# Optimization experiments

Measured on AMD Instinct MI355X. Metric: run time of the kernel, lower is better.

## Reference

```python
import jax, jax.numpy as jnp
import numpy as np

N, R, E, H, F = 50000, 6, 32768, 256, 16
NH, HD = 8, 32
EPS_LN = 1e-5

def _ln(x, g, b):
    mu = x.mean(-1, keepdims=True)
    var = ((x - mu) ** 2).mean(-1, keepdims=True)
    return (x - mu) * jax.lax.rsqrt(var + EPS_LN) * g + b

def setup_inputs() -> dict:
    key = jax.random.key(0)
    ks = jax.random.split(key, 32)
    s = lambda i, shape, scale=0.05: jax.random.normal(ks[i], shape, jnp.float32) * scale
    return {
        'x': jax.random.normal(ks[0], (N, H), jnp.float32),
        'edge_index': jax.random.randint(ks[1], (R, 2, E), 0, N, jnp.int32),
        'edge_attr': jax.random.normal(ks[2], (R, E, F), jnp.float32),
        'Wq': s(3, (R, H, H)), 'bq': s(4, (R, H)),
        'Wk': s(5, (R, H + F, H)), 'bk': s(6, (R, H)),
        'Wv': s(7, (R, H + F, H)), 'bv': s(8, (R, H)),
        'prior': jnp.ones((R, NH), jnp.float32),
        'Wm': s(9, (R, H, H)), 'bm': s(10, (R, H)),
        'W_ir1': s(11, (R * H, H)), 'b_ir1': s(12, (H,)),
        'W_ir2': s(13, (H, R)), 'b_ir2': s(14, (R,)),
        'Wmp': s(15, (3, H, H)), 'bmp': s(16, (3, H)),
        'Wa1': s(17, (H, H // 2)), 'ba1': s(18, (H // 2,)),
        'Wa2': s(19, (H // 2, 1)),
        'g_meta': jnp.ones((H,), jnp.float32), 'b_meta': jnp.zeros((H,), jnp.float32),
        'Wc': s(20, (2 * H, H)), 'bc': s(21, (H,)),
        'g_out': jnp.ones((H,), jnp.float32), 'b_out': jnp.zeros((H,), jnp.float32),
    }

def _block(x, edge_index, edge_attr, Wq, bq, Wk, bk, Wv, bv, prior, Wm, bm,
           W_ir1, b_ir1, W_ir2, b_ir2, Wmp, bmp, Wa1, ba1, Wa2, g_meta, b_meta,
           Wc, bc, g_out, b_out):
    def rel_layer(eidx, eattr, wq, bq_, wk, bk_, wv, bv_, pr, wm, bm_):
        src, dst = eidx[0], eidx[1]
        q = x @ wq + bq_                                  # [N,H]
        kv_in = jnp.concatenate([x[src], eattr], -1)      # [E,H+F]
        k = (kv_in @ wk + bk_).reshape(E, NH, HD)
        v = (kv_in @ wv + bv_).reshape(E, NH, HD)
        qe = q[dst].reshape(E, NH, HD)
        scores = (qe * k).sum(-1) / np.sqrt(HD) * pr      # [E,NH]
        m = jax.ops.segment_max(scores, dst, num_segments=N)
        ex = jnp.exp(scores - m[dst])
        denom = jax.ops.segment_sum(ex, dst, num_segments=N)
        w = ex / (denom[dst] + 1e-16)
        wv_flat = (w[..., None] * v).reshape(E, H)
        agg = jax.ops.segment_sum(wv_flat, dst, num_segments=N)  # [N,H]
        return jax.nn.gelu(agg @ wm + bm_, approximate=False)

    rel_out = jax.vmap(rel_layer)(edge_index, edge_attr, Wq, bq, Wk, bk, Wv, bv,
                                  prior, Wm, bm)          # [R,N,H]

    all_rel = jnp.transpose(rel_out, (1, 0, 2)).reshape(N, R * H)
    h = jax.nn.gelu(all_rel @ W_ir1 + b_ir1, approximate=False)
    inter_w = jax.nn.softmax(h @ W_ir2 + b_ir2, axis=-1)  # [N,R]
    inter_agg = jnp.einsum('nr,rnh->nh', inter_w, rel_out)

    # meta-paths: 0=entangle(ENTANGLE=2,SWAP=3) 1=control(CONTROL=4,ROTATION=0) 2=local(PAULI=1,TEMPORAL=5)
    paths = jnp.stack([rel_out[2] + rel_out[3], rel_out[4] + rel_out[0],
                       rel_out[1] + rel_out[5]], axis=1)  # [N,3,H]
    stacked = jnp.einsum('nph,phk->npk', paths, Wmp) + bmp
    attn = jax.nn.softmax((jnp.tanh(stacked @ Wa1 + ba1) @ Wa2).squeeze(-1), axis=1)
    meta = _ln((attn[..., None] * stacked).sum(1), g_meta, b_meta)

    combined = jax.nn.gelu(jnp.concatenate([inter_agg, meta], -1) @ Wc + bc,
                           approximate=False)
    return _ln(x + combined, g_out, b_out)

def reference(x, edge_index, edge_attr, Wq, bq, Wk, bk, Wv, bv, prior, Wm, bm,
              W_ir1, b_ir1, W_ir2, b_ir2, Wmp, bmp, Wa1, ba1, Wa2, g_meta, b_meta,
              Wc, bc, g_out, b_out):
    return _block(x, edge_index, edge_attr, Wq, bq, Wk, bk, Wv, bv, prior, Wm, bm,
                  W_ir1, b_ir1, W_ir2, b_ir2, Wmp, bmp, Wa1, ba1, Wa2,
                  g_meta, b_meta, Wc, bc, g_out, b_out)
```

## Files before the change

kernel.cpp:

```cpp
#include <hip/hip_runtime.h>
#include <hip/hip_bf16.h>

typedef __hip_bfloat16 bf16;
typedef __attribute__((ext_vector_type(8))) short short8;
typedef __attribute__((ext_vector_type(4))) float f32x4;

#define NN 50000
#define RR 6
#define EE 32768
#define HH 256
#define FF 16
#define NHEAD 8
#define KVP 320

struct __align__(8) bf16x4 { bf16 v[4]; };

__device__ __forceinline__ float b2f(bf16 v) { return __bfloat162float(v); }
__device__ __forceinline__ bf16 f2b(float v) { return __float2bfloat16(v); }
__device__ __forceinline__ short f2s(float f) { bf16 b = f2b(f); return __builtin_bit_cast(short, b); }
__device__ __forceinline__ float s2f(short s) { return b2f(__builtin_bit_cast(bf16, s)); }
__device__ __forceinline__ float gelu_f(float x) { return 0.5f * x * (1.0f + erff(x * 0.7071067811865476f)); }
__device__ __forceinline__ unsigned fkey(float f) { unsigned u = __float_as_uint(f); return (u & 0x80000000u) ? ~u : (u | 0x80000000u); }
__device__ __forceinline__ float fdec(unsigned k) { unsigned u = (k & 0x80000000u) ? (k & 0x7fffffffu) : ~k; return __uint_as_float(u); }

__device__ __forceinline__ void gl2lds16(const void* g, void* l) {
  __builtin_amdgcn_global_load_lds(
      (const __attribute__((address_space(1))) unsigned int*)g,
      (__attribute__((address_space(3))) unsigned int*)l, 16, 0, 0);
}

__global__ void zero_k(uint4* __restrict__ p, int n16)
{
  const uint4 z = make_uint4(0u, 0u, 0u, 0u);
  for (int i = blockIdx.x * blockDim.x + threadIdx.x; i < n16; i += gridDim.x * blockDim.x)
    p[i] = z;
}

__global__ void cvt_k(const float* __restrict__ in, bf16* __restrict__ out, int n4)
{
  const int i = blockIdx.x * 256 + threadIdx.x;
  if (i >= n4) return;
  const float4 f = ((const float4*)in)[i];
  bf16x4 o; o.v[0] = f2b(f.x); o.v[1] = f2b(f.y); o.v[2] = f2b(f.z); o.v[3] = f2b(f.w);
  ((bf16x4*)out)[i] = o;
}

__global__ void tconv_k(const float* __restrict__ in, bf16* __restrict__ out,
                        int K, int NC, int Kp, long izs, long ozs)
{
  __shared__ float t[32][33];
  in  += (size_t)blockIdx.z * izs;
  out += (size_t)blockIdx.z * ozs;
  const int kb = blockIdx.x * 32, nb = blockIdx.y * 32;
  const int tx = threadIdx.x & 31, ty = threadIdx.x >> 5;
  for (int i = ty; i < 32; i += 8) {
    const int k = kb + i, n = nb + tx;
    t[i][tx] = (k < K && n < NC) ? in[(size_t)k * NC + n] : 0.f;
  }
  __syncthreads();
  for (int i = ty; i < 32; i += 8) {
    const int n = nb + i, k = kb + tx;
    if (n < NC && k < Kp) out[(size_t)n * Kp + k] = f2b(t[tx][i]);
  }
}

__global__ void bkv_k(const float* __restrict__ bk, const float* __restrict__ bv,
                      float* __restrict__ bkv)
{
  const int i = blockIdx.x * 256 + threadIdx.x;
  if (i >= RR * 512) return;
  const int r = i >> 9, c = i & 511;
  bkv[i] = (c < 256) ? bk[r * 256 + c] : bv[r * 256 + (c - 256)];
}

__global__ void copyslot_k(const bf16* __restrict__ tmp, bf16* __restrict__ slot)
{
  const int i = blockIdx.x * 256 + threadIdx.x;
  if (i >= NN * 32) return;
  const int n = i >> 5, c = (i & 31) * 8;
  *(short8*)(slot + (size_t)n * 1536 + c) = *(const short8*)(tmp + (size_t)n * 256 + c);
}

template<int ASRC, int ACT, int ZMODE, typename TO>
__global__ __launch_bounds__(256) void mm_k(
    const void* __restrict__ Av, const bf16* __restrict__ A2, int lda,
    const int* __restrict__ src, const float* __restrict__ eattr,
    const bf16* __restrict__ Bt, const float* __restrict__ bias,
    const float* __restrict__ wa2, TO* __restrict__ C, int ldc,
    float* __restrict__ logits, int M, int K, int z0)
{
  __shared__ short lA[128 * 64];
  __shared__ short lB[128 * 64];
  const int tid = threadIdx.x;
  const int w = tid >> 6, l = tid & 63;
  const int col0 = blockIdx.x << 7;
  const int row0 = blockIdx.y << 7;
  const bf16* Ab = (const bf16*)Av;
  const bf16* A2b = A2;
  const bf16* Btz = Bt;
  const float* biasz = bias;
  TO* Cz = C;
  float* lg = logits;
  if constexpr (ZMODE == 1) {
    const int slots3[3] = {2, 4, 1};
    Ab = (const bf16*)Av + slots3[blockIdx.z] * 256;
    lg = logits + (size_t)blockIdx.z * M;
  } else if constexpr (ZMODE == 3) {
    const int r1s[3] = {2, 4, 1}, r2s[3] = {3, 0, 5};
    const int z = blockIdx.z + z0;
    Ab  = (const bf16*)Av + (size_t)r1s[z] * 256;
    A2b = A2 + (size_t)r2s[z] * 256;
    Btz = Bt + (size_t)z * 256 * K;
    biasz = bias + z * 256;
    Cz = C + (size_t)blockIdx.z * (size_t)M * 256;
  }
  const int wm = (w >> 1) << 6, wn = (w & 1) << 6;
  const int lane15 = l & 15, kq = l >> 4;

  f32x4 acc[4][4] = {};

  for (int k0 = 0; k0 < K; k0 += 64) {
#pragma unroll
    for (int i = 0; i < 4; ++i) {
      const int idx = (w * 4 + i) * 64 + l;
      const int row = idx >> 3, cg = idx & 7;
      const int scg = cg ^ (row & 7);
      const int r = min(row0 + row, M - 1);
      const int kc = k0 + scg * 8;
      if constexpr (ASRC == 0) {
        gl2lds16(Ab + (size_t)r * lda + kc, &lA[idx * 8]);
      } else if constexpr (ASRC == 2) {
        const short8 u  = *(const short8*)(Ab + (size_t)r * lda + kc);
        const short8 v2 = *(const short8*)(A2b + (size_t)r * lda + kc);
        short8 s;
#pragma unroll
        for (int j = 0; j < 8; ++j) s[j] = f2s(s2f(u[j]) + s2f(v2[j]));
        *(short8*)&lA[idx * 8] = s;
      } else {
        short8 s;
        if (kc < HH) {
          s = *(const short8*)((const bf16*)Av + (size_t)src[r] * HH + kc);
        } else if (kc < HH + FF) {
          const float* p = eattr + (size_t)r * FF + (kc - HH);
          const float4 f0 = *(const float4*)p;
          const float4 f1 = *(const float4*)(p + 4);
          s[0] = f2s(f0.x); s[1] = f2s(f0.y); s[2] = f2s(f0.z); s[3] = f2s(f0.w);
          s[4] = f2s(f1.x); s[5] = f2s(f1.y); s[6] = f2s(f1.z); s[7] = f2s(f1.w);
        } else {
#pragma unroll
          for (int j = 0; j < 8; ++j) s[j] = 0;
        }
        *(short8*)&lA[idx * 8] = s;
      }
    }
#pragma unroll
    for (int i = 0; i < 4; ++i) {
      const int idx = (w * 4 + i) * 64 + l;
      const int row = idx >> 3, cg = idx & 7;
      const int scg = cg ^ (row & 7);
      gl2lds16(Btz + (size_t)(col0 + row) * K + k0 + scg * 8, &lB[idx * 8]);
    }
    __syncthreads();
#pragma unroll
    for (int kk = 0; kk < 64; kk += 32) {
      short8 af[4], bfr[4];
#pragma unroll
      for (int t = 0; t < 4; ++t) {
        const int ra = wm + t * 16 + lane15;
        const int ca = ((kk >> 3) + kq) ^ (ra & 7);
        af[t] = *(const short8*)&lA[ra * 64 + ca * 8];
        const int rb = wn + t * 16 + lane15;
        const int cb = ((kk >> 3) + kq) ^ (rb & 7);
        bfr[t] = *(const short8*)&lB[rb * 64 + cb * 8];
      }
#pragma unroll
      for (int ti = 0; ti < 4; ++ti)
#pragma unroll
        for (int tj = 0; tj < 4; ++tj)
          acc[ti][tj] = __builtin_amdgcn_mfma_f32_16x16x32_bf16(af[ti], bfr[tj], acc[ti][tj], 0, 0, 0);
    }
    __syncthreads();
  }

  if constexpr (ZMODE != 1) {
#pragma unroll
    for (int ti = 0; ti < 4; ++ti) {
#pragma unroll
      for (int reg = 0; reg < 4; ++reg) {
        const int row = row0 + wm + ti * 16 + kq * 4 + reg;
        if (row >= M) continue;
#pragma unroll
        for (int tj = 0; tj < 4; ++tj) {
          const int col = col0 + wn + tj * 16 + lane15;
          float v = acc[ti][tj][reg] + biasz[col];
          if constexpr (ACT == 1) v = gelu_f(v);
          if constexpr (sizeof(TO) == 2) Cz[(size_t)row * ldc + col] = (TO)f2b(v);
          else                           Cz[(size_t)row * ldc + col] = (TO)v;
        }
      }
    }
  } else {
#pragma unroll
    for (int ti = 0; ti < 4; ++ti) {
#pragma unroll
      for (int reg = 0; reg < 4; ++reg) {
        float part = 0.f;
#pragma unroll
        for (int tj = 0; tj < 4; ++tj) {
          const int col = col0 + wn + tj * 16 + lane15;
          part += tanhf(acc[ti][tj][reg] + biasz[col]) * wa2[col];
        }
#pragma unroll
        for (int off = 8; off > 0; off >>= 1) part += __shfl_xor(part, off, 64);
        const int row = row0 + wm + ti * 16 + kq * 4 + reg;
        if (lane15 == 0 && row < M) atomicAdd(&lg[row], part);
      }
    }
  }
}

__global__ void scores_k(const bf16* __restrict__ q, const bf16* __restrict__ kv,
                         const int* __restrict__ dst_idx, const float* __restrict__ prior_r,
                         float* __restrict__ scores, unsigned* __restrict__ mkey)
{
  const int e = blockIdx.x, t = threadIdx.x;
  const int dst = dst_idx[e];
  float p = b2f(q[(size_t)dst * 1536 + t]) * b2f(kv[(size_t)e * 512 + t]);
#pragma unroll
  for (int off = 16; off > 0; off >>= 1) p += __shfl_down(p, off, 32);
  const int h = t >> 5;
  if ((t & 31) == 0) {
    const float s = p * 0.1767766952966369f * prior_r[h];
    scores[e * NHEAD + h] = s;
    atomicMax(&mkey[dst * NHEAD + h], fkey(s));
  }
}

__global__ void expden_k(const float* __restrict__ scores, const int* __restrict__ dst_idx,
                         const unsigned* __restrict__ mkey, float* __restrict__ ex,
                         float* __restrict__ denom)
{
  const int idx = blockIdx.x * 256 + threadIdx.x;
  if (idx >= EE * NHEAD) return;
  const int e = idx >> 3, h = idx & 7;
  const int dst = dst_idx[e];
  const float m = fdec(mkey[dst * NHEAD + h]);
  const float v = expf(scores[idx] - m);
  ex[idx] = v;
  atomicAdd(&denom[dst * NHEAD + h], v);
}

__global__ void agg_k(const float* __restrict__ ex, const float* __restrict__ denom,
                      const bf16* __restrict__ kv, const int* __restrict__ dst_idx,
                      float* __restrict__ agg)
{
  const int e = blockIdx.x, t = threadIdx.x, h = t >> 5;
  const int dst = dst_idx[e];
  const float w = ex[e * NHEAD + h] / (denom[dst * NHEAD + h] + 1e-16f);
  atomicAdd(&agg[(size_t)dst * HH + t], w * b2f(kv[(size_t)e * 512 + 256 + t]));
}

__global__ void interw_k(const bf16* __restrict__ h, const float* __restrict__ W2,
                         const float* __restrict__ b2, float* __restrict__ interw)
{
  const int wv = threadIdx.x >> 6, ln = threadIdx.x & 63;
  const int n = blockIdx.x * 4 + wv;
  if (n >= NN) return;
  float a[6] = {0.f, 0.f, 0.f, 0.f, 0.f, 0.f};
#pragma unroll
  for (int kq = 0; kq < 4; ++kq) {
    const int k = ln + (kq << 6);
    const float hv = b2f(h[(size_t)n * HH + k]);
#pragma unroll
    for (int j = 0; j < 6; ++j) a[j] += hv * W2[k * 6 + j];
  }
#pragma unroll
  for (int j = 0; j < 6; ++j) {
#pragma unroll
    for (int off = 32; off > 0; off >>= 1) a[j] += __shfl_down(a[j], off, 64);
  }
  if (ln == 0) {
    float lg[6], e[6], mx = -1e30f, s = 0.f;
#pragma unroll
    for (int j = 0; j < 6; ++j) { lg[j] = a[j] + b2[j]; mx = fmaxf(mx, lg[j]); }
#pragma unroll
    for (int j = 0; j < 6; ++j) { e[j] = expf(lg[j] - mx); s += e[j]; }
    const float inv = 1.0f / s;
#pragma unroll
    for (int j = 0; j < 6; ++j) interw[(size_t)n * 6 + j] = e[j] * inv;
  }
}

__global__ void interagg_k(const float* __restrict__ interw, const bf16* __restrict__ rel_cat,
                           bf16* __restrict__ comb)
{
  const int n = blockIdx.x, t = threadIdx.x;
  float acc = 0.f;
#pragma unroll
  for (int r = 0; r < 6; ++r)
    acc += interw[(size_t)n * 6 + r] * b2f(rel_cat[(size_t)n * 1536 + r * 256 + t]);
  comb[(size_t)n * 512 + t] = f2b(acc);
}

__global__ void metafinal_k(const float* __restrict__ logits, const bf16* __restrict__ rel_cat,
                            const float* __restrict__ gmeta, const float* __restrict__ bmeta,
                            bf16* __restrict__ comb)
{
  const int wv = threadIdx.x >> 6, ln = threadIdx.x & 63;
  const int n = blockIdx.x * 4 + wv;
  if (n >= NN) return;
  const float l0 = logits[n], l1 = logits[NN + n], l2 = logits[2 * NN + n];
  const float mx = fmaxf(l0, fmaxf(l1, l2));
  const float e0 = expf(l0 - mx), e1 = expf(l1 - mx), e2 = expf(l2 - mx);
  const float inv = 1.0f / (e0 + e1 + e2);
  const float a0 = e0 * inv, a1 = e1 * inv, a2 = e2 * inv;
  const size_t base = (size_t)n * 1536;
  float pre[4], s = 0.f, s2 = 0.f;
#pragma unroll
  for (int q4 = 0; q4 < 4; ++q4) {
    const int j = ln + (q4 << 6);
    const float v = a0 * b2f(rel_cat[base + 2 * 256 + j])
                  + a1 * b2f(rel_cat[base + 4 * 256 + j])
                  + a2 * b2f(rel_cat[base + 1 * 256 + j]);
    pre[q4] = v; s += v; s2 += v * v;
  }
#pragma unroll
  for (int off = 32; off > 0; off >>= 1) { s += __shfl_down(s, off, 64); s2 += __shfl_down(s2, off, 64); }
  s = __shfl(s, 0, 64); s2 = __shfl(s2, 0, 64);
  const float mu = s * (1.0f / 256.0f);
  const float var = s2 * (1.0f / 256.0f) - mu * mu;
  const float rs = rsqrtf(var + 1e-5f);
#pragma unroll
  for (int q4 = 0; q4 < 4; ++q4) {
    const int j = ln + (q4 << 6);
    comb[(size_t)n * 512 + 256 + j] = f2b((pre[q4] - mu) * rs * gmeta[j] + bmeta[j]);
  }
}

__global__ void final_k(const float* __restrict__ x, const float* __restrict__ combined,
                        const float* __restrict__ g, const float* __restrict__ b,
                        float* __restrict__ out)
{
  __shared__ float sred[8];
  const int n = blockIdx.x, t = threadIdx.x;
  const float v = x[(size_t)n * HH + t] + combined[(size_t)n * HH + t];
  float s = v, s2 = v * v;
#pragma unroll
  for (int off = 32; off > 0; off >>= 1) { s += __shfl_down(s, off, 64); s2 += __shfl_down(s2, off, 64); }
  const int wv = t >> 6;
  if ((t & 63) == 0) { sred[wv] = s; sred[4 + wv] = s2; }
  __syncthreads();
  const float st = sred[0] + sred[1] + sred[2] + sred[3];
  const float st2 = sred[4] + sred[5] + sred[6] + sred[7];
  const float mu = st * (1.0f / 256.0f);
  const float var = st2 * (1.0f / 256.0f) - mu * mu;
  const float rs = rsqrtf(var + 1e-5f);
  out[(size_t)n * HH + t] = (v - mu) * rs * g[t] + b[t];
}

extern "C" void kernel_launch(void* const* d_in, const int* in_sizes, int n_in,
                              void* d_out, int out_size, void* d_ws, size_t ws_size,
                              hipStream_t stream)
{
  const float* x      = (const float*)d_in[0];
  const int*   eidx   = (const int*)d_in[1];
  const float* eattr  = (const float*)d_in[2];
  const float* Wq     = (const float*)d_in[3];
  const float* bq     = (const float*)d_in[4];
  const float* Wk     = (const float*)d_in[5];
  const float* bk     = (const float*)d_in[6];
  const float* Wv     = (const float*)d_in[7];
  const float* bv     = (const float*)d_in[8];
  const float* prior  = (const float*)d_in[9];
  const float* Wm     = (const float*)d_in[10];
  const float* bm     = (const float*)d_in[11];
  const float* W_ir1  = (const float*)d_in[12];
  const float* b_ir1  = (const float*)d_in[13];
  const float* W_ir2  = (const float*)d_in[14];
  const float* b_ir2  = (const float*)d_in[15];
  const float* Wmp    = (const float*)d_in[16];
  const float* bmp    = (const float*)d_in[17];
  const float* Wa1    = (const float*)d_in[18];
  const float* ba1    = (const float*)d_in[19];
  const float* Wa2    = (const float*)d_in[20];
  const float* g_meta = (const float*)d_in[21];
  const float* b_meta = (const float*)d_in[22];
  const float* Wc     = (const float*)d_in[23];
  const float* bc     = (const float*)d_in[24];
  const float* g_out  = (const float*)d_in[25];
  const float* b_out  = (const float*)d_in[26];
  float* out = (float*)d_out;

  char* ws = (char*)d_ws;
  bf16* rel_cat = (bf16*)ws;
  char* W0 = ws + 153600000;
  bf16*  Wqt   = (bf16*)(W0 + 0);
  bf16*  Wkvt  = (bf16*)(W0 + 786432);
  bf16*  Wmt   = (bf16*)(W0 + 2752512);
  bf16*  Wir1t = (bf16*)(W0 + 3538944);
  bf16*  Wct   = (bf16*)(W0 + 4325376);
  bf16*  Wmpt  = (bf16*)(W0 + 4587520);
  bf16*  Wa1t  = (bf16*)(W0 + 4980736);
  float* bkv   = (float*)(W0 + 5046272);
  char* region = ws + 158658560;
  bf16*     kvbuf = (bf16*)(region + 0);
  float*    sc    = (float*)(region + 33554432);
  float*    exb   = (float*)(region + 34603008);
  unsigned* mkey  = (unsigned*)(region + 35651584);
  float*    denom = (float*)(region + 37251584);
  bf16*     xb    = (bf16*)(region + 38851584);
  float*    agg   = out;
  bf16*     aggb  = (bf16*)(region + 0);
  bf16*  hbuf     = (bf16*)(region + 0);
  float* interw   = (float*)(region + 33554432);
  bf16*  tmp      = (bf16*)(region + 0);
  float* logits   = (float*)(region + 51200000);
  bf16*  comb     = (bf16*)out;
  float* combined = (float*)(region + 0);

  const dim3 gN(2, 391);
  const dim3 gQ(12, 391);
  const dim3 gKV(4, 256);
  const dim3 gMP2(2, 391, 2);
  const dim3 gMP1(2, 391, 1);
  const dim3 gL(1, 391, 3);

  tconv_k<<<dim3(8, 8, 6), 256, 0, stream>>>(Wq, Wqt, 256, 256, 256, 256 * 256, 256 * 256);
  tconv_k<<<dim3(10, 8, 6), 256, 0, stream>>>(Wk, Wkvt, 272, 256, 320, 272 * 256, 512 * 320);
  tconv_k<<<dim3(10, 8, 6), 256, 0, stream>>>(Wv, Wkvt + 256 * 320, 272, 256, 320, 272 * 256, 512 * 320);
  tconv_k<<<dim3(8, 8, 6), 256, 0, stream>>>(Wm, Wmt, 256, 256, 256, 256 * 256, 256 * 256);
  tconv_k<<<dim3(48, 8, 1), 256, 0, stream>>>(W_ir1, Wir1t, 1536, 256, 1536, 0, 0);
  tconv_k<<<dim3(16, 8, 1), 256, 0, stream>>>(Wc, Wct, 512, 256, 512, 0, 0);
  tconv_k<<<dim3(8, 8, 3), 256, 0, stream>>>(Wmp, Wmpt, 256, 256, 256, 256 * 256, 256 * 256);
  tconv_k<<<dim3(8, 4, 1), 256, 0, stream>>>(Wa1, Wa1t, 256, 128, 256, 0, 0);
  bkv_k<<<12, 256, 0, stream>>>(bk, bv, bkv);
  cvt_k<<<(NN * 64 + 255) / 256, 256, 0, stream>>>(x, xb, NN * 64);

  mm_k<0, 0, 0, bf16><<<gQ, 256, 0, stream>>>(
      xb, nullptr, 256, nullptr, nullptr,
      Wqt, bq, nullptr, rel_cat, 1536, nullptr, NN, 256, 0);

  for (int r = 0; r < RR; ++r) {
    const int* src = eidx + (size_t)r * 2 * EE;
    const int* dst = src + EE;
    const float* ea = eattr + (size_t)r * EE * FF;
    zero_k<<<391, 256, 0, stream>>>((uint4*)mkey, (2 * NN * NHEAD * 4) / 16);
    zero_k<<<2048, 256, 0, stream>>>((uint4*)agg, (NN * HH * 4) / 16);
    mm_k<3, 0, 0, bf16><<<gKV, 256, 0, stream>>>(
        xb, nullptr, 0, src, ea,
        Wkvt + (size_t)r * 512 * KVP, bkv + r * 512, nullptr, kvbuf, 512, nullptr, EE, KVP, 0);
    scores_k<<<EE, 256, 0, stream>>>(rel_cat + r * 256, kvbuf, dst, prior + r * NHEAD, sc, mkey);
    expden_k<<<(EE * NHEAD + 255) / 256, 256, 0, stream>>>(sc, dst, mkey, exb, denom);
    agg_k<<<EE, 256, 0, stream>>>(exb, denom, kvbuf, dst, agg);
    cvt_k<<<(NN * 64 + 255) / 256, 256, 0, stream>>>(agg, (bf16*)aggb, NN * 64);
    mm_k<0, 1, 0, bf16><<<gN, 256, 0, stream>>>(
        aggb, nullptr, 256, nullptr, nullptr,
        Wmt + (size_t)r * 256 * 256, bm + r * HH, nullptr,
        rel_cat + r * 256, 1536, nullptr, NN, 256, 0);
  }

  mm_k<0, 1, 0, bf16><<<gN, 256, 0, stream>>>(
      rel_cat, nullptr, 1536, nullptr, nullptr,
      Wir1t, b_ir1, nullptr, hbuf, 256, nullptr, NN, 1536, 0);
  interw_k<<<(NN + 3) / 4, 256, 0, stream>>>(hbuf, W_ir2, b_ir2, interw);
  interagg_k<<<NN, 256, 0, stream>>>(interw, rel_cat, comb);

  mm_k<2, 0, 3, bf16><<<gMP2, 256, 0, stream>>>(
      rel_cat, rel_cat, 1536, nullptr, nullptr,
      Wmpt, bmp, nullptr, tmp, 256, nullptr, NN, 256, 0);
  copyslot_k<<<(NN * 32 + 255) / 256, 256, 0, stream>>>(tmp, rel_cat + 2 * 256);
  copyslot_k<<<(NN * 32 + 255) / 256, 256, 0, stream>>>(tmp + (size_t)NN * 256, rel_cat + 4 * 256);
  mm_k<2, 0, 3, bf16><<<gMP1, 256, 0, stream>>>(
      rel_cat, rel_cat, 1536, nullptr, nullptr,
      Wmpt, bmp, nullptr, tmp, 256, nullptr, NN, 256, 2);
  copyslot_k<<<(NN * 32 + 255) / 256, 256, 0, stream>>>(tmp, rel_cat + 1 * 256);

  zero_k<<<147, 256, 0, stream>>>((uint4*)logits, (3 * NN * 4) / 16);
  mm_k<0, 0, 1, bf16><<<gL, 256, 0, stream>>>(
      rel_cat, nullptr, 1536, nullptr, nullptr,
      Wa1t, ba1, Wa2, (bf16*)nullptr, 0, logits, NN, 256, 0);
  metafinal_k<<<(NN + 3) / 4, 256, 0, stream>>>(logits, rel_cat, g_meta, b_meta, comb);

  mm_k<0, 1, 0, float><<<gN, 256, 0, stream>>>(
      comb, nullptr, 512, nullptr, nullptr,
      Wct, bc, nullptr, combined, 256, nullptr, NN, 512, 0);
  final_k<<<NN, 256, 0, stream>>>(x, combined, g_out, b_out, out);
}
```

Before: 1.599 ms.

## Fuse edge softmax into single pass without max subtraction; normalize in GEMM load

Replaces the scores/segment-max, exp/denominator and aggregation kernels with one edge kernel that computes exp(score) directly and atomically accumulates both the denominator and the unnormalized weighted values. The division by the denominator and the fp32-to-bf16 conversion move into the A-tile load of the following GEMM, which removes the separate convert pass. Edge attributes are converted to bf16 once up front. Dropping the max subtraction removes two passes and the intermediate buffers, but exp can overflow for large scores.

```diff
diff --git a/kernel.cpp b/kernel.cpp
--- a/kernel.cpp
+++ b/kernel.cpp
@@ -20,8 +20,6 @@
 __device__ __forceinline__ short f2s(float f) { bf16 b = f2b(f); return __builtin_bit_cast(short, b); }
 __device__ __forceinline__ float s2f(short s) { return b2f(__builtin_bit_cast(bf16, s)); }
 __device__ __forceinline__ float gelu_f(float x) { return 0.5f * x * (1.0f + erff(x * 0.7071067811865476f)); }
-__device__ __forceinline__ unsigned fkey(float f) { unsigned u = __float_as_uint(f); return (u & 0x80000000u) ? ~u : (u | 0x80000000u); }
-__device__ __forceinline__ float fdec(unsigned k) { unsigned u = (k & 0x80000000u) ? (k & 0x7fffffffu) : ~k; return __uint_as_float(u); }
 
 __device__ __forceinline__ void gl2lds16(const void* g, void* l) {
   __builtin_amdgcn_global_load_lds(
@@ -84,7 +82,8 @@
 template<int ASRC, int ACT, int ZMODE, typename TO>
 __global__ __launch_bounds__(256) void mm_k(
     const void* __restrict__ Av, const bf16* __restrict__ A2, int lda,
-    const int* __restrict__ src, const float* __restrict__ eattr,
+    const int* __restrict__ src, const bf16* __restrict__ eab,
+    const float* __restrict__ dnm,
     const bf16* __restrict__ Bt, const float* __restrict__ bias,
     const float* __restrict__ wa2, TO* __restrict__ C, int ldc,
     float* __restrict__ logits, int M, int K, int z0)
@@ -130,26 +129,31 @@
       if constexpr (ASRC == 0) {
         gl2lds16(Ab + (size_t)r * lda + kc, &lA[idx * 8]);
       } else if constexpr (ASRC == 2) {
-        const short8 u  = *(const short8*)(Ab + (size_t)r * lda + kc);
+        const short8 u  = *(const short8*)(Ab  + (size_t)r * lda + kc);
         const short8 v2 = *(const short8*)(A2b + (size_t)r * lda + kc);
         short8 s;
 #pragma unroll
         for (int j = 0; j < 8; ++j) s[j] = f2s(s2f(u[j]) + s2f(v2[j]));
         *(short8*)&lA[idx * 8] = s;
-      } else {
+      } else if constexpr (ASRC == 3) {
         short8 s;
         if (kc < HH) {
           s = *(const short8*)((const bf16*)Av + (size_t)src[r] * HH + kc);
         } else if (kc < HH + FF) {
-          const float* p = eattr + (size_t)r * FF + (kc - HH);
-          const float4 f0 = *(const float4*)p;
-          const float4 f1 = *(const float4*)(p + 4);
-          s[0] = f2s(f0.x); s[1] = f2s(f0.y); s[2] = f2s(f0.z); s[3] = f2s(f0.w);
-          s[4] = f2s(f1.x); s[5] = f2s(f1.y); s[6] = f2s(f1.z); s[7] = f2s(f1.w);
+          s = *(const short8*)(eab + (size_t)r * FF + (kc - HH));
         } else {
 #pragma unroll
           for (int j = 0; j < 8; ++j) s[j] = 0;
         }
+        *(short8*)&lA[idx * 8] = s;
+      } else {
+        const float* p = (const float*)Av + (size_t)r * lda + kc;
+        const float4 f0 = *(const float4*)p;
+        const float4 f1 = *(const float4*)(p + 4);
+        const float iv = 1.0f / (dnm[r * NHEAD + (kc >> 5)] + 1e-16f);
+        short8 s;
+        s[0] = f2s(f0.x * iv); s[1] = f2s(f0.y * iv); s[2] = f2s(f0.z * iv); s[3] = f2s(f0.w * iv);
+        s[4] = f2s(f1.x * iv); s[5] = f2s(f1.y * iv); s[6] = f2s(f1.z * iv); s[7] = f2s(f1.w * iv);
         *(short8*)&lA[idx * 8] = s;
       }
     }
@@ -219,45 +223,20 @@
   }
 }
 
-__global__ void scores_k(const bf16* __restrict__ q, const bf16* __restrict__ kv,
-                         const int* __restrict__ dst_idx, const float* __restrict__ prior_r,
-                         float* __restrict__ scores, unsigned* __restrict__ mkey)
+__global__ void edge_k(const bf16* __restrict__ q, const bf16* __restrict__ kv,
+                       const int* __restrict__ dst_idx, const float* __restrict__ prior_r,
+                       float* __restrict__ denom, float* __restrict__ agg)
 {
   const int e = blockIdx.x, t = threadIdx.x;
   const int dst = dst_idx[e];
+  const int h = t >> 5;
   float p = b2f(q[(size_t)dst * 1536 + t]) * b2f(kv[(size_t)e * 512 + t]);
 #pragma unroll
   for (int off = 16; off > 0; off >>= 1) p += __shfl_down(p, off, 32);
-  const int h = t >> 5;
-  if ((t & 31) == 0) {
-    const float s = p * 0.1767766952966369f * prior_r[h];
-    scores[e * NHEAD + h] = s;
-    atomicMax(&mkey[dst * NHEAD + h], fkey(s));
-  }
-}
-
-__global__ void expden_k(const float* __restrict__ scores, const int* __restrict__ dst_idx,
-                         const unsigned* __restrict__ mkey, float* __restrict__ ex,
-                         float* __restrict__ denom)
-{
-  const int idx = blockIdx.x * 256 + threadIdx.x;
-  if (idx >= EE * NHEAD) return;
-  const int e = idx >> 3, h = idx & 7;
-  const int dst = dst_idx[e];
-  const float m = fdec(mkey[dst * NHEAD + h]);
-  const float v = expf(scores[idx] - m);
-  ex[idx] = v;
-  atomicAdd(&denom[dst * NHEAD + h], v);
-}
-
-__global__ void agg_k(const float* __restrict__ ex, const float* __restrict__ denom,
-                      const bf16* __restrict__ kv, const int* __restrict__ dst_idx,
-                      float* __restrict__ agg)
-{
-  const int e = blockIdx.x, t = threadIdx.x, h = t >> 5;
-  const int dst = dst_idx[e];
-  const float w = ex[e * NHEAD + h] / (denom[dst * NHEAD + h] + 1e-16f);
-  atomicAdd(&agg[(size_t)dst * HH + t], w * b2f(kv[(size_t)e * 512 + 256 + t]));
+  const float s = __shfl(p, 0, 32);
+  const float ex = expf(s * 0.1767766952966369f * prior_r[h]);
+  if ((t & 31) == 0) atomicAdd(&denom[dst * NHEAD + h], ex);
+  atomicAdd(&agg[(size_t)dst * HH + t], ex * b2f(kv[(size_t)e * 512 + 256 + t]));
 }
 
 __global__ void interw_k(const bf16* __restrict__ h, const float* __restrict__ W2,
@@ -404,13 +383,10 @@
   float* bkv   = (float*)(W0 + 5046272);
   char* region = ws + 158658560;
   bf16*     kvbuf = (bf16*)(region + 0);
-  float*    sc    = (float*)(region + 33554432);
-  float*    exb   = (float*)(region + 34603008);
-  unsigned* mkey  = (unsigned*)(region + 35651584);
-  float*    denom = (float*)(region + 37251584);
+  float*    denom = (float*)(region + 33554432);
   bf16*     xb    = (bf16*)(region + 38851584);
+  bf16*     eab   = (bf16*)(region + 64451584);
   float*    agg   = out;
-  bf16*     aggb  = (bf16*)(region + 0);
   bf16*  hbuf     = (bf16*)(region + 0);
   float* interw   = (float*)(region + 33554432);
   bf16*  tmp      = (bf16*)(region + 0);
@@ -435,54 +411,51 @@
   tconv_k<<<dim3(8, 4, 1), 256, 0, stream>>>(Wa1, Wa1t, 256, 128, 256, 0, 0);
   bkv_k<<<12, 256, 0, stream>>>(bk, bv, bkv);
   cvt_k<<<(NN * 64 + 255) / 256, 256, 0, stream>>>(x, xb, NN * 64);
+  cvt_k<<<(RR * EE * FF / 4 + 255) / 256, 256, 0, stream>>>(eattr, eab, RR * EE * FF / 4);
 
   mm_k<0, 0, 0, bf16><<<gQ, 256, 0, stream>>>(
-      xb, nullptr, 256, nullptr, nullptr,
+      xb, nullptr, 256, nullptr, nullptr, nullptr,
       Wqt, bq, nullptr, rel_cat, 1536, nullptr, NN, 256, 0);
 
   for (int r = 0; r < RR; ++r) {
     const int* src = eidx + (size_t)r * 2 * EE;
     const int* dst = src + EE;
-    const float* ea = eattr + (size_t)r * EE * FF;
-    zero_k<<<391, 256, 0, stream>>>((uint4*)mkey, (2 * NN * NHEAD * 4) / 16);
+    zero_k<<<98, 256, 0, stream>>>((uint4*)denom, (NN * NHEAD * 4) / 16);
     zero_k<<<2048, 256, 0, stream>>>((uint4*)agg, (NN * HH * 4) / 16);
     mm_k<3, 0, 0, bf16><<<gKV, 256, 0, stream>>>(
-        xb, nullptr, 0, src, ea,
+        xb, nullptr, 0, src, eab + (size_t)r * EE * FF, nullptr,
         Wkvt + (size_t)r * 512 * KVP, bkv + r * 512, nullptr, kvbuf, 512, nullptr, EE, KVP, 0);
-    scores_k<<<EE, 256, 0, stream>>>(rel_cat + r * 256, kvbuf, dst, prior + r * NHEAD, sc, mkey);
-    expden_k<<<(EE * NHEAD + 255) / 256, 256, 0, stream>>>(sc, dst, mkey, exb, denom);
-    agg_k<<<EE, 256, 0, stream>>>(exb, denom, kvbuf, dst, agg);
-    cvt_k<<<(NN * 64 + 255) / 256, 256, 0, stream>>>(agg, (bf16*)aggb, NN * 64);
-    mm_k<0, 1, 0, bf16><<<gN, 256, 0, stream>>>(
-        aggb, nullptr, 256, nullptr, nullptr,
+    edge_k<<<EE, 256, 0, stream>>>(rel_cat + r * 256, kvbuf, dst, prior + r * NHEAD, denom, agg);
+    mm_k<4, 1, 0, bf16><<<gN, 256, 0, stream>>>(
+        agg, nullptr, 256, nullptr, nullptr, denom,
         Wmt + (size_t)r * 256 * 256, bm + r * HH, nullptr,
         rel_cat + r * 256, 1536, nullptr, NN, 256, 0);
   }
 
   mm_k<0, 1, 0, bf16><<<gN, 256, 0, stream>>>(
-      rel_cat, nullptr, 1536, nullptr, nullptr,
+      rel_cat, nullptr, 1536, nullptr, nullptr, nullptr,
       Wir1t, b_ir1, nullptr, hbuf, 256, nullptr, NN, 1536, 0);
   interw_k<<<(NN + 3) / 4, 256, 0, stream>>>(hbuf, W_ir2, b_ir2, interw);
   interagg_k<<<NN, 256, 0, stream>>>(interw, rel_cat, comb);
 
   mm_k<2, 0, 3, bf16><<<gMP2, 256, 0, stream>>>(
-      rel_cat, rel_cat, 1536, nullptr, nullptr,
+      rel_cat, rel_cat, 1536, nullptr, nullptr, nullptr,
       Wmpt, bmp, nullptr, tmp, 256, nullptr, NN, 256, 0);
   copyslot_k<<<(NN * 32 + 255) / 256, 256, 0, stream>>>(tmp, rel_cat + 2 * 256);
   copyslot_k<<<(NN * 32 + 255) / 256, 256, 0, stream>>>(tmp + (size_t)NN * 256, rel_cat + 4 * 256);
   mm_k<2, 0, 3, bf16><<<gMP1, 256, 0, stream>>>(
-      rel_cat, rel_cat, 1536, nullptr, nullptr,
+      rel_cat, rel_cat, 1536, nullptr, nullptr, nullptr,
       Wmpt, bmp, nullptr, tmp, 256, nullptr, NN, 256, 2);
   copyslot_k<<<(NN * 32 + 255) / 256, 256, 0, stream>>>(tmp, rel_cat + 1 * 256);
 
   zero_k<<<147, 256, 0, stream>>>((uint4*)logits, (3 * NN * 4) / 16);
   mm_k<0, 0, 1, bf16><<<gL, 256, 0, stream>>>(
-      rel_cat, nullptr, 1536, nullptr, nullptr,
+      rel_cat, nullptr, 1536, nullptr, nullptr, nullptr,
       Wa1t, ba1, Wa2, (bf16*)nullptr, 0, logits, NN, 256, 0);
   metafinal_k<<<(NN + 3) / 4, 256, 0, stream>>>(logits, rel_cat, g_meta, b_meta, comb);
 
   mm_k<0, 1, 0, float><<<gN, 256, 0, stream>>>(
-      comb, nullptr, 512, nullptr, nullptr,
+      comb, nullptr, 512, nullptr, nullptr, nullptr,
       Wct, bc, nullptr, combined, 256, nullptr, NN, 512, 0);
   final_k<<<NN, 256, 0, stream>>>(x, combined, g_out, b_out, out);
 }
```

Result: faster. 1.442 ms (-9.8%).
